# Optimization experiments

Hardware: AMD Instinct MI355X
Metric: run time of the kernel (lower is better)

## Reference

```python
import jax, jax.numpy as jnp
import numpy as np
import math

B, A, D = 32, 100, 10000
HID = 256
NH = 4
OUT = 10000
NFREQ = 16
E = round(OUT * 0.5 / (A / 2))  # max_entries = 100
N = int(math.sqrt(D))           # 100 (row/col decode of flat index)
SCALE = math.sqrt(HID)
STEPS = 3


def swish(x):
    return x * jax.nn.sigmoid(x)


def setup_inputs() -> dict:
    key = jax.random.key(0)
    ks = jax.random.split(key, 16)
    s = 0.02
    p = lambda k, shape: jax.random.normal(k, shape, jnp.float32) * s
    vals = jax.random.normal(ks[0], (B, A, D), jnp.float32)
    keep = jax.random.uniform(ks[1], (B, A, D)) < (E / D)  # ~E nonzeros per (b, agent)
    x = vals * keep
    return {
        "x": x,
        "fourier_B": jax.random.normal(ks[2], (NFREQ, 2), jnp.float32),
        "enc_W1": p(ks[3], (HID, 1 + 2 * NFREQ)), "enc_b1": jnp.zeros((HID,), jnp.float32),
        "enc_W2": p(ks[4], (HID, HID)), "enc_b2": jnp.zeros((HID,), jnp.float32),
        "pad_token": jnp.zeros((HID,), jnp.float32),
        "comp_W1": p(ks[5], (2 * HID, E * HID)), "comp_b1": jnp.zeros((2 * HID,), jnp.float32),
        "comp_W2": p(ks[6], (HID, 2 * HID)), "comp_b2": jnp.zeros((HID,), jnp.float32),
        "connectivity": jax.random.normal(ks[7], (A, A), jnp.float32),
        "qW": p(ks[8], (NH, HID, HID)), "kW": p(ks[9], (NH, HID, HID)), "vW": p(ks[10], (NH, HID, HID)),
        "fp_W1": p(ks[11], (NH, HID, HID)), "fp_b1": jnp.zeros((NH, HID), jnp.float32),
        "fp_W2": p(ks[12], (NH, HID, HID)), "fp_b2": jnp.zeros((NH, HID), jnp.float32),
        "ln_g": jnp.ones((NH, HID), jnp.float32), "ln_b": jnp.zeros((NH, HID), jnp.float32),
        "out_W": p(ks[13], (OUT, HID)), "out_b": jnp.zeros((OUT,), jnp.float32),
    }


def reference(x, fourier_B, enc_W1, enc_b1, enc_W2, enc_b2, pad_token,
              comp_W1, comp_b1, comp_W2, comp_b2, connectivity,
              qW, kW, vW, fp_W1, fp_b1, fp_W2, fp_b2, ln_g, ln_b, out_W, out_b):
    # --- ragged gather of nonzero entries, truncated/padded to E per (b, agent) ---
    mask = x != 0                                                   # [B,A,D]
    # stable argsort puts nonzero positions first, in ascending flat-index order
    # (same order as torch .nonzero per batch row)
    idx = jnp.argsort(jnp.logical_not(mask), axis=-1, stable=True)[..., :E]  # [B,A,E]
    valid = jnp.take_along_axis(mask, idx, axis=-1)                 # [B,A,E]
    vals = jnp.take_along_axis(x, idx, axis=-1)[..., None]          # [B,A,E,1]
    coords = jnp.stack([idx // N, idx % N], axis=-1).astype(x.dtype)  # [B,A,E,2]
    # Fourier positional encoding
    proj = (2.0 * math.pi) * jnp.einsum('baec,fc->baef', coords, fourier_B)
    pos = jnp.concatenate([jnp.sin(proj), jnp.cos(proj)], axis=-1)  # [B,A,E,2F]
    feat = jnp.concatenate([vals, pos], axis=-1)                    # [B,A,E,1+2F]
    # entry encoder MLP
    e = swish(feat @ enc_W1.T + enc_b1) @ enc_W2.T + enc_b2         # [B,A,E,HID]
    e = jnp.where(valid[..., None], e, pad_token)                   # pad slots -> pad_token
    # per-agent compression of the E entry embeddings
    flat = e.reshape(B, A, E * HID)
    h = swish(flat @ comp_W1.T + comp_b1) @ comp_W2.T + comp_b2     # [B,A,HID]

    # --- message passing: multi-head dot-product GAT with learned connectivity bias ---
    conn = connectivity[None, None]                                  # broadcast [1,1,A,A]
    for _ in range(STEPS):
        Q = jnp.einsum('bai,nji->nbaj', h, qW)                      # [NH,B,A,HID]
        K = jnp.einsum('bai,nji->nbaj', h, kW)
        V = jnp.einsum('bai,nji->nbaj', h, vW)
        scores = jnp.einsum('nbaj,nbcj->nbac', Q, K) / SCALE + conn
        alpha = jax.nn.softmax(scores, axis=-1)                     # dropout p=0.0
        Hm = jnp.einsum('nbac,nbcj->nbaj', alpha, V)
        t = jnp.einsum('nbaj,nij->nbai', swish(Hm), fp_W1) + fp_b1[:, None, None, :]
        t = jnp.einsum('nbaj,nij->nbai', swish(t), fp_W2) + fp_b2[:, None, None, :]
        m = t.mean(-1, keepdims=True)
        v = ((t - m) ** 2).mean(-1, keepdims=True)
        o = (t - m) / jnp.sqrt(v + 1e-5) * ln_g[:, None, None, :] + ln_b[:, None, None, :]
        h = o.mean(0)                                               # mean over heads

    return h @ out_W.T + out_b                                      # [B,A,OUT]
```

## Files before the change

kernel.cpp:

```cpp
#include <hip/hip_runtime.h>
#include <cstdint>
#include <cstddef>

#define NBATCH 32
#define NAGENT 100
#define NDIM   10000
#define HID    256
#define NHEAD  4
#define NOUT   10000
#define NFREQ  16
#define EMAX   100
#define NBA    3200
#define KBIG   25600
#define TWO_PI 6.283185307179586476925f

typedef float  v4f  __attribute__((ext_vector_type(4)));
typedef short  v8s  __attribute__((ext_vector_type(8)));

__device__ __forceinline__ unsigned short bf_hi(float f) {
    unsigned int u = __float_as_uint(f);
    return (unsigned short)((u + 0x7FFFu + ((u >> 16) & 1u)) >> 16);
}
__device__ __forceinline__ float bf_tof(unsigned short h) {
    return __uint_as_float(((unsigned int)h) << 16);
}

__global__ __launch_bounds__(64) void k_extract(const float* __restrict__ x,
                                                int* __restrict__ idxb,
                                                float* __restrict__ valb,
                                                int* __restrict__ nvalid)
{
    const int ba = blockIdx.x;
    const float* xr = x + (size_t)ba * NDIM;
    const int lane = threadIdx.x;
    int base = 0;
    for (int c0 = 0; c0 < NDIM; c0 += 64) {
        int i = c0 + lane;
        float v = (i < NDIM) ? xr[i] : 0.0f;
        unsigned long long m = __ballot(v != 0.0f);
        if (v != 0.0f) {
            int p = base + __popcll(m & ((1ull << lane) - 1ull));
            if (p < EMAX) {
                idxb[(size_t)ba * EMAX + p] = i;
                valb[(size_t)ba * EMAX + p] = v;
            }
        }
        base += __popcll(m);
        if (base >= EMAX) break;
    }
    if (lane == 0) nvalid[ba] = base < EMAX ? base : EMAX;
}

__global__ __launch_bounds__(256) void k_g1(
    const int* __restrict__ idxb, const float* __restrict__ valb,
    const int* __restrict__ nvalid, const float* __restrict__ fourB,
    const float* __restrict__ W1, const float* __restrict__ b1,
    unsigned short* __restrict__ g1h, unsigned short* __restrict__ g1l)
{
    __shared__ float s_feat[16][36];
    __shared__ float s_w[8448];
    __shared__ float s_b1v[256];
    __shared__ int   s_idx[16];
    __shared__ int   s_valid[16];

    const int t  = threadIdx.x;
    const int g0 = blockIdx.x * 16;

    if (t < 16) {
        int g = g0 + t;
        int ba = g / 100, slot = g - ba * 100;
        int valid = (slot < nvalid[ba]) ? 1 : 0;
        s_valid[t]   = valid;
        s_idx[t]     = valid ? idxb[g] : 0;
        s_feat[t][0] = valid ? valb[g] : 0.0f;
    }
    s_b1v[t] = b1[t];
    for (int i = t; i < 8448; i += 256) s_w[i] = W1[i];
    __syncthreads();

    {
        int ent = t >> 4, f = t & 15;
        float sv = 0.0f, cv = 0.0f;
        if (s_valid[ent]) {
            int id = s_idx[ent];
            float row = (float)(id / 100);
            float col = (float)(id % 100);
            float pr = TWO_PI * (row * fourB[2 * f] + col * fourB[2 * f + 1]);
            sv = sinf(pr); cv = cosf(pr);
        }
        s_feat[ent][1 + f]  = sv;
        s_feat[ent][17 + f] = cv;
    }
    __syncthreads();

    const float* wr = &s_w[t * 33];
    for (int ent = 0; ent < 16; ++ent) {
        float a = s_b1v[t];
        #pragma unroll
        for (int c = 0; c < 33; ++c) a += s_feat[ent][c] * wr[c];
        float g = a / (1.0f + expf(-a));
        g = s_valid[ent] ? g : 0.0f;
        unsigned short h = bf_hi(g);
        unsigned short l = bf_hi(g - bf_tof(h));
        size_t o = (size_t)(g0 + ent) * 256 + t;
        g1h[o] = h;
        g1l[o] = l;
    }
}

__global__ void k_w2t(const float* __restrict__ W2, float* __restrict__ W2T)
{
    int kp = blockIdx.x, k = threadIdx.x;
    W2T[kp * 256 + k] = W2[k * 256 + kp];
}

__global__ __launch_bounds__(256) void k_wsplit(const float* __restrict__ src,
                                                unsigned short* __restrict__ hi,
                                                unsigned short* __restrict__ lo)
{
    int i = (blockIdx.x * 256 + threadIdx.x) * 4;
    float4 f = *(const float4*)(src + i);
    ushort4 h, l;
    h.x = bf_hi(f.x); l.x = bf_hi(f.x - bf_tof(h.x));
    h.y = bf_hi(f.y); l.y = bf_hi(f.y - bf_tof(h.y));
    h.z = bf_hi(f.z); l.z = bf_hi(f.z - bf_tof(h.z));
    h.w = bf_hi(f.w); l.w = bf_hi(f.w - bf_tof(h.w));
    *(ushort4*)(hi + i) = h;
    *(ushort4*)(lo + i) = l;
}

__global__ __launch_bounds__(256) void k_tables(
    const float* __restrict__ W1, const float* __restrict__ pad,
    const float* __restrict__ b2, float* __restrict__ D, float* __restrict__ E0)
{
    __shared__ float red[4];
    const int n = blockIdx.x;
    const int t = threadIdx.x, lane = t & 63, w = t >> 6;
    const float pm = pad[t] - b2[t];
    const float bb = b2[t];
    const float* wr = W1 + (size_t)n * KBIG;
    float eb = 0.0f;
    for (int s = 0; s < 100; ++s) {
        float wv = wr[s * 256 + t];
        float p = pm * wv;
        eb += bb * wv;
        #pragma unroll
        for (int o = 32; o > 0; o >>= 1) p += __shfl_down(p, o);
        if (lane == 0) red[w] = p;
        __syncthreads();
        if (t == 0) D[s * 512 + n] = red[0] + red[1] + red[2] + red[3];
        __syncthreads();
    }
    #pragma unroll
    for (int o = 32; o > 0; o >>= 1) eb += __shfl_down(eb, o);
    if (lane == 0) red[w] = eb;
    __syncthreads();
    if (t == 0) E0[n] = red[0] + red[1] + red[2] + red[3];
}

__global__ void k_suffix(const float* __restrict__ D, float* __restrict__ Corr)
{
    int n = blockIdx.x * 256 + threadIdx.x;
    float c = 0.0f;
    Corr[100 * 512 + n] = 0.0f;
    for (int s = 99; s >= 0; --s) { c += D[s * 512 + n]; Corr[s * 512 + n] = c; }
}

template<int ACT, int SPLIT>
__global__ __launch_bounds__(256) void k_gemmbf(
    const unsigned short* __restrict__ Ah, const unsigned short* __restrict__ Al,
    const unsigned short* __restrict__ Wh, const unsigned short* __restrict__ Wl,
    const float* __restrict__ bias, float* __restrict__ C,
    unsigned short* __restrict__ Ch, unsigned short* __restrict__ Cl,
    int M, int N, int K,
    long long sA, long long sW, long long sBias, long long sC)
{
    __shared__ unsigned short sA_h[4096], sA_l[4096], sW_h[4096], sW_l[4096];
    const int t = threadIdx.x;
    const int z = blockIdx.z;
    Ah += (size_t)z * sA;  Al += (size_t)z * sA;
    Wh += (size_t)z * sW;  Wl += (size_t)z * sW;
    if (SPLIT) { Ch += (size_t)z * sC; Cl += (size_t)z * sC; }
    else       { C  += (size_t)z * sC; }
    const float* bp = bias ? (bias + (size_t)z * sBias) : nullptr;
    const int bn = blockIdx.x * 128, bm = blockIdx.y * 128;
    const int lane = t & 63, w = t >> 6;
    const int wm = (w & 1) * 64, wn = (w >> 1) * 64;
    const int r0 = t >> 2, kq = (t & 3) * 8;
    const int r1 = 64 + r0;
    const uint4 zero4 = make_uint4(0u, 0u, 0u, 0u);

    const unsigned short* pA0 = Ah + (size_t)(bm + r0) * K + kq;
    const unsigned short* pA1 = Ah + (size_t)(bm + r1) * K + kq;
    const unsigned short* pa0 = Al + (size_t)(bm + r0) * K + kq;
    const unsigned short* pa1 = Al + (size_t)(bm + r1) * K + kq;
    const bool v0 = (bn + r0) < N, v1 = (bn + r1) < N;
    const unsigned short* pW0 = Wh + (size_t)(bn + r0) * K + kq;
    const unsigned short* pW1 = Wh + (size_t)(bn + r1) * K + kq;
    const unsigned short* pw0 = Wl + (size_t)(bn + r0) * K + kq;
    const unsigned short* pw1 = Wl + (size_t)(bn + r1) * K + kq;

    uint4 rA0 = *(const uint4*)pA0, rA1 = *(const uint4*)pA1;
    uint4 ra0 = *(const uint4*)pa0, ra1 = *(const uint4*)pa1;
    uint4 rW0 = v0 ? *(const uint4*)pW0 : zero4;
    uint4 rW1 = v1 ? *(const uint4*)pW1 : zero4;
    uint4 rw0 = v0 ? *(const uint4*)pw0 : zero4;
    uint4 rw1 = v1 ? *(const uint4*)pw1 : zero4;

    v4f acc[4][4] = {};
    const int i0 = (r0 * 32 + kq) ^ ((r0 & 7) << 3);
    const int i1 = (r1 * 32 + kq) ^ ((r1 & 7) << 3);
    const int KT = K >> 5;

    for (int kt = 0; kt < KT; ++kt) {
        __syncthreads();
        *(uint4*)&sA_h[i0] = rA0;  *(uint4*)&sA_h[i1] = rA1;
        *(uint4*)&sA_l[i0] = ra0;  *(uint4*)&sA_l[i1] = ra1;
        *(uint4*)&sW_h[i0] = rW0;  *(uint4*)&sW_h[i1] = rW1;
        *(uint4*)&sW_l[i0] = rw0;  *(uint4*)&sW_l[i1] = rw1;
        __syncthreads();
        if (kt + 1 < KT) {
            int o = (kt + 1) * 32;
            rA0 = *(const uint4*)(pA0 + o);  rA1 = *(const uint4*)(pA1 + o);
            ra0 = *(const uint4*)(pa0 + o);  ra1 = *(const uint4*)(pa1 + o);
            rW0 = v0 ? *(const uint4*)(pW0 + o) : zero4;
            rW1 = v1 ? *(const uint4*)(pW1 + o) : zero4;
            rw0 = v0 ? *(const uint4*)(pw0 + o) : zero4;
            rw1 = v1 ? *(const uint4*)(pw1 + o) : zero4;
        }
        const int fr = lane & 15, fq = (lane >> 4) * 8;
        v8s ahf[4], alf[4], bhf[4], blf[4];
        #pragma unroll
        for (int i = 0; i < 4; ++i) {
            int ar = wm + i * 16 + fr;
            int br = wn + i * 16 + fr;
            int ai = (ar * 32 + fq) ^ ((ar & 7) << 3);
            int bi = (br * 32 + fq) ^ ((br & 7) << 3);
            ahf[i] = *(const v8s*)&sA_h[ai];
            alf[i] = *(const v8s*)&sA_l[ai];
            bhf[i] = *(const v8s*)&sW_h[bi];
            blf[i] = *(const v8s*)&sW_l[bi];
        }
        #pragma unroll
        for (int mi = 0; mi < 4; ++mi)
            #pragma unroll
            for (int ni = 0; ni < 4; ++ni) {
                acc[mi][ni] = __builtin_amdgcn_mfma_f32_16x16x32_bf16(ahf[mi], bhf[ni], acc[mi][ni], 0, 0, 0);
                acc[mi][ni] = __builtin_amdgcn_mfma_f32_16x16x32_bf16(ahf[mi], blf[ni], acc[mi][ni], 0, 0, 0);
                acc[mi][ni] = __builtin_amdgcn_mfma_f32_16x16x32_bf16(alf[mi], bhf[ni], acc[mi][ni], 0, 0, 0);
            }
    }

    const int er = (lane >> 4) * 4, ec = lane & 15;
    #pragma unroll
    for (int mi = 0; mi < 4; ++mi)
        #pragma unroll
        for (int ni = 0; ni < 4; ++ni) {
            int m = bm + wm + mi * 16 + er;
            int n = bn + wn + ni * 16 + ec;
            if (n < N) {
                float bv = bp ? bp[n] : 0.0f;
                #pragma unroll
                for (int r = 0; r < 4; ++r) {
                    float val = acc[mi][ni][r] + bv;
                    if (ACT == 1) val = val / (1.0f + expf(-val));
                    if (SPLIT) {
                        unsigned short hv = bf_hi(val);
                        Ch[(size_t)(m + r) * N + n] = hv;
                        Cl[(size_t)(m + r) * N + n] = bf_hi(val - bf_tof(hv));
                    } else {
                        C[(size_t)(m + r) * N + n] = val;
                    }
                }
            }
        }
    (void)M;
}

__global__ __launch_bounds__(256) void k_g3mfma(
    const unsigned short* __restrict__ Ah, const unsigned short* __restrict__ Al,
    const unsigned short* __restrict__ Wh, const unsigned short* __restrict__ Wl,
    float* __restrict__ part)
{
    __shared__ unsigned short sAh[4096], sAl[4096], sWh[4096], sWl[4096];
    const int t  = threadIdx.x;
    const int hwid = blockIdx.x;
    const int wk = (hwid & 7) * 100 + (hwid >> 3);
    const int bn = (wk & 3) * 128;
    const int bm = ((wk >> 2) % 25) * 128;
    const int z  = wk / 100;
    const int lane = t & 63, w = t >> 6;
    const int wm = (w & 1) * 64, wn = (w >> 1) * 64;
    const size_t K = KBIG;
    const int r0 = t >> 2, kq = (t & 3) * 8;
    const int r1 = 64 + r0;

    const unsigned short* pA0 = Ah + (size_t)(bm + r0) * K + z * 3200 + kq;
    const unsigned short* pA1 = Ah + (size_t)(bm + r1) * K + z * 3200 + kq;
    const unsigned short* pa0 = Al + (size_t)(bm + r0) * K + z * 3200 + kq;
    const unsigned short* pa1 = Al + (size_t)(bm + r1) * K + z * 3200 + kq;
    const unsigned short* pW0 = Wh + (size_t)(bn + r0) * K + z * 3200 + kq;
    const unsigned short* pW1 = Wh + (size_t)(bn + r1) * K + z * 3200 + kq;
    const unsigned short* pw0 = Wl + (size_t)(bn + r0) * K + z * 3200 + kq;
    const unsigned short* pw1 = Wl + (size_t)(bn + r1) * K + z * 3200 + kq;

    uint4 rA0 = *(const uint4*)pA0, rA1 = *(const uint4*)pA1;
    uint4 ra0 = *(const uint4*)pa0, ra1 = *(const uint4*)pa1;
    uint4 rW0 = *(const uint4*)pW0, rW1 = *(const uint4*)pW1;
    uint4 rw0 = *(const uint4*)pw0, rw1 = *(const uint4*)pw1;

    v4f acc[4][4] = {};
    const int i0 = (r0 * 32 + kq) ^ ((r0 & 7) << 3);
    const int i1 = (r1 * 32 + kq) ^ ((r1 & 7) << 3);

    for (int kt = 0; kt < 100; ++kt) {
        __syncthreads();
        *(uint4*)&sAh[i0] = rA0;  *(uint4*)&sAh[i1] = rA1;
        *(uint4*)&sAl[i0] = ra0;  *(uint4*)&sAl[i1] = ra1;
        *(uint4*)&sWh[i0] = rW0;  *(uint4*)&sWh[i1] = rW1;
        *(uint4*)&sWl[i0] = rw0;  *(uint4*)&sWl[i1] = rw1;
        __syncthreads();
        if (kt < 99) {
            int off = (kt + 1) * 32;
            rA0 = *(const uint4*)(pA0 + off);  rA1 = *(const uint4*)(pA1 + off);
            ra0 = *(const uint4*)(pa0 + off);  ra1 = *(const uint4*)(pa1 + off);
            rW0 = *(const uint4*)(pW0 + off);  rW1 = *(const uint4*)(pW1 + off);
            rw0 = *(const uint4*)(pw0 + off);  rw1 = *(const uint4*)(pw1 + off);
        }
        const int fr = lane & 15, fq = (lane >> 4) * 8;
        v8s ah[4], al[4], bh[4], bl[4];
        #pragma unroll
        for (int i = 0; i < 4; ++i) {
            int ar = wm + i * 16 + fr;
            int br = wn + i * 16 + fr;
            int ai = (ar * 32 + fq) ^ ((ar & 7) << 3);
            int bi = (br * 32 + fq) ^ ((br & 7) << 3);
            ah[i] = *(const v8s*)&sAh[ai];
            al[i] = *(const v8s*)&sAl[ai];
            bh[i] = *(const v8s*)&sWh[bi];
            bl[i] = *(const v8s*)&sWl[bi];
        }
        #pragma unroll
        for (int mi = 0; mi < 4; ++mi)
            #pragma unroll
            for (int ni = 0; ni < 4; ++ni) {
                acc[mi][ni] = __builtin_amdgcn_mfma_f32_16x16x32_bf16(ah[mi], bh[ni], acc[mi][ni], 0, 0, 0);
                acc[mi][ni] = __builtin_amdgcn_mfma_f32_16x16x32_bf16(ah[mi], bl[ni], acc[mi][ni], 0, 0, 0);
                acc[mi][ni] = __builtin_amdgcn_mfma_f32_16x16x32_bf16(al[mi], bh[ni], acc[mi][ni], 0, 0, 0);
            }
    }

    const int er = (lane >> 4) * 4, ec = lane & 15;
    float* cp = part + (size_t)z * NBA * 512;
    #pragma unroll
    for (int mi = 0; mi < 4; ++mi)
        #pragma unroll
        for (int ni = 0; ni < 4; ++ni) {
            int m = bm + wm + mi * 16 + er;
            int n = bn + wn + ni * 16 + ec;
            #pragma unroll
            for (int r = 0; r < 4; ++r)
                cp[(size_t)(m + r) * 512 + n] = acc[mi][ni][r];
        }
}

__global__ __launch_bounds__(256) void k_g3red(
    const float* __restrict__ part, const float* __restrict__ comp_b1,
    const float* __restrict__ E0, const float* __restrict__ Corr,
    const int* __restrict__ nvalid,
    unsigned short* __restrict__ oh, unsigned short* __restrict__ ol)
{
    const int i4 = (blockIdx.x * 256 + threadIdx.x) * 4;
    const int ba = i4 >> 9, n = i4 & 511;
    const size_t S = (size_t)NBA * 512;
    float4 s = *(const float4*)(part + i4);
    #pragma unroll
    for (int zz = 1; zz < 8; ++zz) {
        float4 p = *(const float4*)(part + zz * S + i4);
        s.x += p.x; s.y += p.y; s.z += p.z; s.w += p.w;
    }
    int nv = nvalid[ba];
    float4 b  = *(const float4*)(comp_b1 + n);
    float4 e  = *(const float4*)(E0 + n);
    float4 c  = *(const float4*)(Corr + nv * 512 + n);
    float r0 = s.x + b.x + e.x + c.x;
    float r1 = s.y + b.y + e.y + c.y;
    float r2 = s.z + b.z + e.z + c.z;
    float r3 = s.w + b.w + e.w + c.w;
    float4 o;
    o.x = r0 / (1.0f + expf(-r0));
    o.y = r1 / (1.0f + expf(-r1));
    o.z = r2 / (1.0f + expf(-r2));
    o.w = r3 / (1.0f + expf(-r3));
    ushort4 h, l;
    h.x = bf_hi(o.x); l.x = bf_hi(o.x - bf_tof(h.x));
    h.y = bf_hi(o.y); l.y = bf_hi(o.y - bf_tof(h.y));
    h.z = bf_hi(o.z); l.z = bf_hi(o.z - bf_tof(h.z));
    h.w = bf_hi(o.w); l.w = bf_hi(o.w - bf_tof(h.w));
    *(ushort4*)(oh + i4) = h;
    *(ushort4*)(ol + i4) = l;
}

__global__ __launch_bounds__(256) void k_attn(
    const float* __restrict__ Qb, const float* __restrict__ Kb,
    const float* __restrict__ Vb, const float* __restrict__ conn,
    unsigned short* __restrict__ Oh, unsigned short* __restrict__ Ol)
{
    __shared__ float sKV[256][101];
    __shared__ float sAl[50][100];
    __shared__ float sQ[2][256];
    __shared__ float sRed[2][2];

    const int t = threadIdx.x;
    const int half = blockIdx.x, b = blockIdx.y, n = blockIdx.z;
    const size_t base = ((size_t)n * NBA + b * 100) * 256;

    const float* Kp = Kb + base;
    for (int r = 0; r < 100; ++r) sKV[t][r] = Kp[(size_t)r * 256 + t];
    __syncthreads();

    const float* Qp = Qb + base;
    const int pair = t >> 7, tt = t & 127, lane = t & 63, wvi = t >> 6;

    for (int rr = 0; rr < 25; ++rr) {
        const int row0 = half * 50 + rr * 2;
        const int lr = rr * 2 + pair;
        __syncthreads();
        sQ[0][t] = Qp[(size_t)(row0)*256 + t];
        sQ[1][t] = Qp[(size_t)(row0 + 1) * 256 + t];
        __syncthreads();
        float sc = 0.0f;
        if (tt < 100) {
            const float* qr = sQ[pair];
            float p0 = 0.f, p1 = 0.f, p2 = 0.f, p3 = 0.f;
            #pragma unroll 4
            for (int c = 0; c < 256; c += 4) {
                p0 += qr[c]     * sKV[c][tt];
                p1 += qr[c + 1] * sKV[c + 1][tt];
                p2 += qr[c + 2] * sKV[c + 2][tt];
                p3 += qr[c + 3] * sKV[c + 3][tt];
            }
            sc = ((p0 + p1) + (p2 + p3)) * 0.0625f + conn[(row0 + pair) * 100 + tt];
            sAl[lr][tt] = sc;
        }
        __syncthreads();
        if ((wvi & 1) == 0) {
            int p = wvi >> 1;
            int r2 = rr * 2 + p;
            float m = sAl[r2][lane];
            if (lane < 36) m = fmaxf(m, sAl[r2][lane + 64]);
            #pragma unroll
            for (int off = 32; off > 0; off >>= 1)
                m = fmaxf(m, __shfl_down(m, off));
            if (lane == 0) sRed[0][p] = m;
        }
        __syncthreads();
        float ex = 0.0f;
        if (tt < 100) {
            ex = expf(sc - sRed[0][pair]);
            sAl[lr][tt] = ex;
        }
        __syncthreads();
        if ((wvi & 1) == 0) {
            int p = wvi >> 1;
            int r2 = rr * 2 + p;
            float s = sAl[r2][lane];
            if (lane < 36) s += sAl[r2][lane + 64];
            #pragma unroll
            for (int off = 32; off > 0; off >>= 1)
                s += __shfl_down(s, off);
            if (lane == 0) sRed[1][p] = s;
        }
        __syncthreads();
        if (tt < 100) sAl[lr][tt] = ex / sRed[1][pair];
    }
    __syncthreads();

    const float* Vp = Vb + base;
    for (int r = 0; r < 100; ++r) sKV[t][r] = Vp[(size_t)r * 256 + t];
    __syncthreads();

    for (int rr = 0; rr < 50; ++rr) {
        int row = half * 50 + rr;
        float a = 0.0f;
        #pragma unroll 4
        for (int j = 0; j < 100; ++j) a += sAl[rr][j] * sKV[t][j];
        float sw = a / (1.0f + expf(-a));
        size_t oidx = base + (size_t)row * 256 + t;
        unsigned short hv = bf_hi(sw);
        Oh[oidx] = hv;
        Ol[oidx] = bf_hi(sw - bf_tof(hv));
    }
}

__global__ __launch_bounds__(256) void k_ln_mean(
    const float* __restrict__ t2b, const float* __restrict__ ln_g,
    const float* __restrict__ ln_b,
    unsigned short* __restrict__ hh, unsigned short* __restrict__ hl)
{
    __shared__ float so[4][256];
    const int ba = blockIdx.x, t = threadIdx.x;
    const int n = t >> 6, lane = t & 63;
    const float* tr = t2b + ((size_t)n * NBA + ba) * HID;
    float4 v = *(const float4*)(tr + lane * 4);
    float s1 = v.x + v.y + v.z + v.w;
    float s2 = v.x * v.x + v.y * v.y + v.z * v.z + v.w * v.w;
    #pragma unroll
    for (int off = 32; off > 0; off >>= 1) {
        s1 += __shfl_down(s1, off);
        s2 += __shfl_down(s2, off);
    }
    s1 = __shfl(s1, 0);
    s2 = __shfl(s2, 0);
    float m = s1 * (1.0f / 256.0f);
    float var = s2 * (1.0f / 256.0f) - m * m;
    float rstd = 1.0f / sqrtf(var + 1e-5f);
    float4 gv = *(const float4*)(ln_g + n * HID + lane * 4);
    float4 bv = *(const float4*)(ln_b + n * HID + lane * 4);
    float4 o;
    o.x = (v.x - m) * rstd * gv.x + bv.x;
    o.y = (v.y - m) * rstd * gv.y + bv.y;
    o.z = (v.z - m) * rstd * gv.z + bv.z;
    o.w = (v.w - m) * rstd * gv.w + bv.w;
    *(float4*)&so[n][lane * 4] = o;
    __syncthreads();
    float hv = 0.25f * (so[0][t] + so[1][t] + so[2][t] + so[3][t]);
    unsigned short hi = bf_hi(hv);
    size_t oidx = (size_t)ba * HID + t;
    hh[oidx] = hi;
    hl[oidx] = bf_hi(hv - bf_tof(hi));
}

extern "C" void kernel_launch(void* const* d_in, const int* in_sizes, int n_in,
                              void* d_out, int out_size, void* d_ws, size_t ws_size,
                              hipStream_t stream)
{
    const float* x       = (const float*)d_in[0];
    const float* fourB   = (const float*)d_in[1];
    const float* enc_W1  = (const float*)d_in[2];
    const float* enc_b1  = (const float*)d_in[3];
    const float* enc_W2  = (const float*)d_in[4];
    const float* enc_b2  = (const float*)d_in[5];
    const float* pad_tok = (const float*)d_in[6];
    const float* comp_W1 = (const float*)d_in[7];
    const float* comp_b1 = (const float*)d_in[8];
    const float* comp_W2 = (const float*)d_in[9];
    const float* comp_b2 = (const float*)d_in[10];
    const float* conn    = (const float*)d_in[11];
    const float* qW      = (const float*)d_in[12];
    const float* kW      = (const float*)d_in[13];
    const float* vW      = (const float*)d_in[14];
    const float* fpW1    = (const float*)d_in[15];
    const float* fpb1    = (const float*)d_in[16];
    const float* fpW2    = (const float*)d_in[17];
    const float* fpb2    = (const float*)d_in[18];
    const float* ln_g    = (const float*)d_in[19];
    const float* ln_b    = (const float*)d_in[20];
    const float* out_W   = (const float*)d_in[21];
    const float* out_b   = (const float*)d_in[22];
    float* outp = (float*)d_out;

    char* ws = (char*)d_ws;
    size_t off = 0;
    auto alloc = [&](size_t bytes) -> void* {
        void* p = (void*)(ws + off);
        off += (bytes + 255) & ~(size_t)255;
        return p;
    };
    int*   idxb = (int*)  alloc((size_t)NBA * EMAX * 4);
    float* valb = (float*)alloc((size_t)NBA * EMAX * 4);
    int*   nval = (int*)  alloc((size_t)NBA * 4);
    unsigned short* g1h = (unsigned short*)alloc((size_t)NBA * KBIG * 2);
    unsigned short* g1l = (unsigned short*)alloc((size_t)NBA * KBIG * 2);
    float* W2T  = (float*)alloc((size_t)256 * 256 * 4);
    float* W1p  = (float*)alloc((size_t)512 * KBIG * 4);
    float* part = W1p;
    unsigned short* Whi = (unsigned short*)alloc((size_t)512 * KBIG * 2);
    unsigned short* Wlo = (unsigned short*)alloc((size_t)512 * KBIG * 2);
    float* Dt   = (float*)alloc((size_t)100 * 512 * 4);
    float* Corr = (float*)alloc((size_t)101 * 512 * 4);
    float* E0   = (float*)alloc((size_t)512 * 4);
    float* Qb   = (float*)alloc((size_t)NHEAD * NBA * HID * 4);
    float* Kb   = (float*)alloc((size_t)NHEAD * NBA * HID * 4);
    float* Vb   = (float*)alloc((size_t)NHEAD * NBA * HID * 4);
    unsigned short* asplh = (unsigned short*)alloc((size_t)NHEAD * NBA * HID * 2);
    unsigned short* aspll = (unsigned short*)alloc((size_t)NHEAD * NBA * HID * 2);
    unsigned short* cW1h = (unsigned short*)Qb;
    unsigned short* cW1l = (unsigned short*)Vb;
    unsigned short* bsplh = g1h;
    unsigned short* bspll = g1h + (size_t)NHEAD * NBA * HID;
    unsigned short* w2tH = (unsigned short*)alloc((size_t)256 * 256 * 2);
    unsigned short* w2tL = (unsigned short*)alloc((size_t)256 * 256 * 2);
    unsigned short* qkvWh = (unsigned short*)alloc((size_t)3 * NHEAD * HID * HID * 2);
    unsigned short* qkvWl = (unsigned short*)alloc((size_t)3 * NHEAD * HID * HID * 2);
    unsigned short* f1Wh = (unsigned short*)alloc((size_t)NHEAD * HID * HID * 2);
    unsigned short* f1Wl = (unsigned short*)alloc((size_t)NHEAD * HID * HID * 2);
    unsigned short* f2Wh = (unsigned short*)alloc((size_t)NHEAD * HID * HID * 2);
    unsigned short* f2Wl = (unsigned short*)alloc((size_t)NHEAD * HID * HID * 2);
    unsigned short* c2Wh = (unsigned short*)alloc((size_t)HID * 512 * 2);
    unsigned short* c2Wl = (unsigned short*)alloc((size_t)HID * 512 * 2);
    unsigned short* oWh  = (unsigned short*)alloc((size_t)NOUT * HID * 2);
    unsigned short* oWl  = (unsigned short*)alloc((size_t)NOUT * HID * 2);
    float* t2b  = Vb;

    const long long sW = (long long)HID * HID;
    const long long sC = (long long)NBA * HID;

    k_extract<<<NBA, 64, 0, stream>>>(x, idxb, valb, nval);
    k_g1<<<NBA * EMAX / 16, 256, 0, stream>>>(idxb, valb, nval, fourB,
                                              enc_W1, enc_b1, g1h, g1l);

    k_w2t<<<256, 256, 0, stream>>>(enc_W2, W2T);
    k_wsplit<<<256 * 256 / 1024, 256, 0, stream>>>(W2T, w2tH, w2tL);
    k_wsplit<<<512 * KBIG / 1024, 256, 0, stream>>>(comp_W1, cW1h, cW1l);
    k_gemmbf<0, 0><<<dim3(2, 400, 1), 256, 0, stream>>>(
        cW1h, cW1l, w2tH, w2tL, nullptr, W1p, nullptr, nullptr,
        512 * EMAX, 256, 256, 0, 0, 0, 0);
    k_wsplit<<<512 * KBIG / 1024, 256, 0, stream>>>(W1p, Whi, Wlo);
    k_tables<<<512, 256, 0, stream>>>(comp_W1, pad_tok, enc_b2, Dt, E0);
    k_suffix<<<2, 256, 0, stream>>>(Dt, Corr);

    k_wsplit<<<NHEAD * 65536 / 1024, 256, 0, stream>>>(qW, qkvWh, qkvWl);
    k_wsplit<<<NHEAD * 65536 / 1024, 256, 0, stream>>>(kW, qkvWh + NHEAD * 65536, qkvWl + NHEAD * 65536);
    k_wsplit<<<NHEAD * 65536 / 1024, 256, 0, stream>>>(vW, qkvWh + 2 * NHEAD * 65536, qkvWl + 2 * NHEAD * 65536);
    k_wsplit<<<NHEAD * 65536 / 1024, 256, 0, stream>>>(fpW1, f1Wh, f1Wl);
    k_wsplit<<<NHEAD * 65536 / 1024, 256, 0, stream>>>(fpW2, f2Wh, f2Wl);
    k_wsplit<<<HID * 512 / 1024, 256, 0, stream>>>(comp_W2, c2Wh, c2Wl);
    k_wsplit<<<NOUT * HID / 1024, 256, 0, stream>>>(out_W, oWh, oWl);

    k_g3mfma<<<800, 256, 0, stream>>>(g1h, g1l, Whi, Wlo, part);
    k_g3red<<<NBA * 512 / 1024, 256, 0, stream>>>(part, comp_b1, E0, Corr, nval, asplh, aspll);
    k_gemmbf<0, 1><<<dim3(2, 25, 1), 256, 0, stream>>>(
        asplh, aspll, c2Wh, c2Wl, comp_b2, nullptr, bsplh, bspll,
        NBA, HID, 512, 0, 0, 0, 0);

    for (int step = 0; step < 3; ++step) {
        k_gemmbf<0, 0><<<dim3(2, 25, 12), 256, 0, stream>>>(
            bsplh, bspll, qkvWh, qkvWl, nullptr, Qb, nullptr, nullptr,
            NBA, HID, HID, 0, sW, 0, sC);
        k_attn<<<dim3(2, NBATCH, NHEAD), 256, 0, stream>>>(Qb, Kb, Vb, conn, asplh, aspll);
        k_gemmbf<1, 1><<<dim3(2, 25, 4), 256, 0, stream>>>(
            asplh, aspll, f1Wh, f1Wl, fpb1, nullptr, bsplh, bspll,
            NBA, HID, HID, sC, sW, HID, sC);
        k_gemmbf<0, 0><<<dim3(2, 25, 4), 256, 0, stream>>>(
            bsplh, bspll, f2Wh, f2Wl, fpb2, t2b, nullptr, nullptr,
            NBA, HID, HID, sC, sW, HID, sC);
        k_ln_mean<<<NBA, 256, 0, stream>>>(t2b, ln_g, ln_b, bsplh, bspll);
    }

    k_gemmbf<0, 0><<<dim3(79, 25, 1), 256, 0, stream>>>(
        bsplh, bspll, oWh, oWl, out_b, outp, nullptr, nullptr,
        NBA, NOUT, HID, 0, 0, 0, 0);

    (void)in_sizes; (void)n_in; (void)out_size; (void)ws_size;
}
```

Before: 1.905 ms.

## Use direct global-to-LDS loads with double buffering in bf16 GEMM kernels

Replaces the register-staged global loads and LDS stores in both split-bf16 GEMM kernels with global_load_lds direct transfers into a double-buffered shared tile. The next K-tile is issued while the current one is consumed, and only one barrier per iteration remains. This aims to cut VGPR pressure and LDS-store instructions and to overlap memory with MFMA work. In exchange it doubles LDS use to 64KB and drops the XOR swizzle, which risks lower occupancy and bank conflicts on fragment reads.

```diff
diff --git a/kernel.cpp b/kernel.cpp
--- a/kernel.cpp
+++ b/kernel.cpp
@@ -23,6 +23,12 @@
 }
 __device__ __forceinline__ float bf_tof(unsigned short h) {
     return __uint_as_float(((unsigned int)h) << 16);
+}
+
+__device__ __forceinline__ void gld16(const void* g, void* l) {
+    __builtin_amdgcn_global_load_lds(
+        (const __attribute__((address_space(1))) void*)g,
+        (__attribute__((address_space(3))) void*)l, 16, 0, 0);
 }
 
 __global__ __launch_bounds__(64) void k_extract(const float* __restrict__ x,
@@ -175,7 +181,7 @@
     int M, int N, int K,
     long long sA, long long sW, long long sBias, long long sC)
 {
-    __shared__ unsigned short sA_h[4096], sA_l[4096], sW_h[4096], sW_l[4096];
+    __shared__ unsigned short lds[2][4][4096];
     const int t = threadIdx.x;
     const int z = blockIdx.z;
     Ah += (size_t)z * sA;  Al += (size_t)z * sA;
@@ -186,60 +192,44 @@
     const int bn = blockIdx.x * 128, bm = blockIdx.y * 128;
     const int lane = t & 63, w = t >> 6;
     const int wm = (w & 1) * 64, wn = (w >> 1) * 64;
-    const int r0 = t >> 2, kq = (t & 3) * 8;
-    const int r1 = 64 + r0;
-    const uint4 zero4 = make_uint4(0u, 0u, 0u, 0u);
-
-    const unsigned short* pA0 = Ah + (size_t)(bm + r0) * K + kq;
-    const unsigned short* pA1 = Ah + (size_t)(bm + r1) * K + kq;
-    const unsigned short* pa0 = Al + (size_t)(bm + r0) * K + kq;
-    const unsigned short* pa1 = Al + (size_t)(bm + r1) * K + kq;
-    const bool v0 = (bn + r0) < N, v1 = (bn + r1) < N;
-    const unsigned short* pW0 = Wh + (size_t)(bn + r0) * K + kq;
-    const unsigned short* pW1 = Wh + (size_t)(bn + r1) * K + kq;
-    const unsigned short* pw0 = Wl + (size_t)(bn + r0) * K + kq;
-    const unsigned short* pw1 = Wl + (size_t)(bn + r1) * K + kq;
-
-    uint4 rA0 = *(const uint4*)pA0, rA1 = *(const uint4*)pA1;
-    uint4 ra0 = *(const uint4*)pa0, ra1 = *(const uint4*)pa1;
-    uint4 rW0 = v0 ? *(const uint4*)pW0 : zero4;
-    uint4 rW1 = v1 ? *(const uint4*)pW1 : zero4;
-    uint4 rw0 = v0 ? *(const uint4*)pw0 : zero4;
-    uint4 rw1 = v1 ? *(const uint4*)pw1 : zero4;
+
+    const int sr = w * 16 + (lane >> 2);
+    const int so = (lane & 3) * 8;
+    int rw0 = bn + sr;       if (rw0 >= N) rw0 = N - 1;
+    int rw1 = bn + 64 + sr;  if (rw1 >= N) rw1 = N - 1;
+    const unsigned short* gA0 = Ah + (size_t)(bm + sr) * K + so;
+    const unsigned short* gA1 = Ah + (size_t)(bm + 64 + sr) * K + so;
+    const unsigned short* ga0 = Al + (size_t)(bm + sr) * K + so;
+    const unsigned short* ga1 = Al + (size_t)(bm + 64 + sr) * K + so;
+    const unsigned short* gW0 = Wh + (size_t)rw0 * K + so;
+    const unsigned short* gW1 = Wh + (size_t)rw1 * K + so;
+    const unsigned short* gw0 = Wl + (size_t)rw0 * K + so;
+    const unsigned short* gw1 = Wl + (size_t)rw1 * K + so;
+    const int lb0 = w * 512;
+    const int lb1 = 2048 + w * 512;
 
     v4f acc[4][4] = {};
-    const int i0 = (r0 * 32 + kq) ^ ((r0 & 7) << 3);
-    const int i1 = (r1 * 32 + kq) ^ ((r1 & 7) << 3);
+    const int fr = lane & 15, fq = (lane >> 4) * 8;
     const int KT = K >> 5;
 
+#define STAGE_G(buf, o)                                                        \
+    gld16(gA0 + (o), &lds[buf][0][lb0]); gld16(gA1 + (o), &lds[buf][0][lb1]);  \
+    gld16(ga0 + (o), &lds[buf][1][lb0]); gld16(ga1 + (o), &lds[buf][1][lb1]);  \
+    gld16(gW0 + (o), &lds[buf][2][lb0]); gld16(gW1 + (o), &lds[buf][2][lb1]);  \
+    gld16(gw0 + (o), &lds[buf][3][lb0]); gld16(gw1 + (o), &lds[buf][3][lb1]);
+
+    STAGE_G(0, 0);
+    __syncthreads();
+    int cur = 0;
     for (int kt = 0; kt < KT; ++kt) {
-        __syncthreads();
-        *(uint4*)&sA_h[i0] = rA0;  *(uint4*)&sA_h[i1] = rA1;
-        *(uint4*)&sA_l[i0] = ra0;  *(uint4*)&sA_l[i1] = ra1;
-        *(uint4*)&sW_h[i0] = rW0;  *(uint4*)&sW_h[i1] = rW1;
-        *(uint4*)&sW_l[i0] = rw0;  *(uint4*)&sW_l[i1] = rw1;
-        __syncthreads();
-        if (kt + 1 < KT) {
-            int o = (kt + 1) * 32;
-            rA0 = *(const uint4*)(pA0 + o);  rA1 = *(const uint4*)(pA1 + o);
-            ra0 = *(const uint4*)(pa0 + o);  ra1 = *(const uint4*)(pa1 + o);
-            rW0 = v0 ? *(const uint4*)(pW0 + o) : zero4;
-            rW1 = v1 ? *(const uint4*)(pW1 + o) : zero4;
-            rw0 = v0 ? *(const uint4*)(pw0 + o) : zero4;
-            rw1 = v1 ? *(const uint4*)(pw1 + o) : zero4;
-        }
-        const int fr = lane & 15, fq = (lane >> 4) * 8;
+        if (kt + 1 < KT) { STAGE_G(cur ^ 1, (kt + 1) * 32); }
         v8s ahf[4], alf[4], bhf[4], blf[4];
         #pragma unroll
         for (int i = 0; i < 4; ++i) {
-            int ar = wm + i * 16 + fr;
-            int br = wn + i * 16 + fr;
-            int ai = (ar * 32 + fq) ^ ((ar & 7) << 3);
-            int bi = (br * 32 + fq) ^ ((br & 7) << 3);
-            ahf[i] = *(const v8s*)&sA_h[ai];
-            alf[i] = *(const v8s*)&sA_l[ai];
-            bhf[i] = *(const v8s*)&sW_h[bi];
-            blf[i] = *(const v8s*)&sW_l[bi];
+            ahf[i] = *(const v8s*)&lds[cur][0][(wm + i * 16 + fr) * 32 + fq];
+            alf[i] = *(const v8s*)&lds[cur][1][(wm + i * 16 + fr) * 32 + fq];
+            bhf[i] = *(const v8s*)&lds[cur][2][(wn + i * 16 + fr) * 32 + fq];
+            blf[i] = *(const v8s*)&lds[cur][3][(wn + i * 16 + fr) * 32 + fq];
         }
         #pragma unroll
         for (int mi = 0; mi < 4; ++mi)
@@ -249,7 +239,10 @@
                 acc[mi][ni] = __builtin_amdgcn_mfma_f32_16x16x32_bf16(ahf[mi], blf[ni], acc[mi][ni], 0, 0, 0);
                 acc[mi][ni] = __builtin_amdgcn_mfma_f32_16x16x32_bf16(alf[mi], bhf[ni], acc[mi][ni], 0, 0, 0);
             }
-    }
+        __syncthreads();
+        cur ^= 1;
+    }
+#undef STAGE_G
 
     const int er = (lane >> 4) * 4, ec = lane & 15;
     #pragma unroll
@@ -282,7 +275,7 @@
     const unsigned short* __restrict__ Wh, const unsigned short* __restrict__ Wl,
     float* __restrict__ part)
 {
-    __shared__ unsigned short sAh[4096], sAl[4096], sWh[4096], sWl[4096];
+    __shared__ unsigned short lds[2][4][4096];
     const int t  = threadIdx.x;
     const int hwid = blockIdx.x;
     const int wk = (hwid & 7) * 100 + (hwid >> 3);
@@ -292,53 +285,41 @@
     const int lane = t & 63, w = t >> 6;
     const int wm = (w & 1) * 64, wn = (w >> 1) * 64;
     const size_t K = KBIG;
-    const int r0 = t >> 2, kq = (t & 3) * 8;
-    const int r1 = 64 + r0;
-
-    const unsigned short* pA0 = Ah + (size_t)(bm + r0) * K + z * 3200 + kq;
-    const unsigned short* pA1 = Ah + (size_t)(bm + r1) * K + z * 3200 + kq;
-    const unsigned short* pa0 = Al + (size_t)(bm + r0) * K + z * 3200 + kq;
-    const unsigned short* pa1 = Al + (size_t)(bm + r1) * K + z * 3200 + kq;
-    const unsigned short* pW0 = Wh + (size_t)(bn + r0) * K + z * 3200 + kq;
-    const unsigned short* pW1 = Wh + (size_t)(bn + r1) * K + z * 3200 + kq;
-    const unsigned short* pw0 = Wl + (size_t)(bn + r0) * K + z * 3200 + kq;
-    const unsigned short* pw1 = Wl + (size_t)(bn + r1) * K + z * 3200 + kq;
-
-    uint4 rA0 = *(const uint4*)pA0, rA1 = *(const uint4*)pA1;
-    uint4 ra0 = *(const uint4*)pa0, ra1 = *(const uint4*)pa1;
-    uint4 rW0 = *(const uint4*)pW0, rW1 = *(const uint4*)pW1;
-    uint4 rw0 = *(const uint4*)pw0, rw1 = *(const uint4*)pw1;
+
+    const int sr = w * 16 + (lane >> 2);
+    const int so = (lane & 3) * 8;
+    const size_t zo = (size_t)z * 3200 + so;
+    const unsigned short* gA0 = Ah + (size_t)(bm + sr) * K + zo;
+    const unsigned short* gA1 = Ah + (size_t)(bm + 64 + sr) * K + zo;
+    const unsigned short* ga0 = Al + (size_t)(bm + sr) * K + zo;
+    const unsigned short* ga1 = Al + (size_t)(bm + 64 + sr) * K + zo;
+    const unsigned short* gW0 = Wh + (size_t)(bn + sr) * K + zo;
+    const unsigned short* gW1 = Wh + (size_t)(bn + 64 + sr) * K + zo;
+    const unsigned short* gw0 = Wl + (size_t)(bn + sr) * K + zo;
+    const unsigned short* gw1 = Wl + (size_t)(bn + 64 + sr) * K + zo;
+    const int lb0 = w * 512, lb1 = 2048 + w * 512;
 
     v4f acc[4][4] = {};
-    const int i0 = (r0 * 32 + kq) ^ ((r0 & 7) << 3);
-    const int i1 = (r1 * 32 + kq) ^ ((r1 & 7) << 3);
-
+    const int fr = lane & 15, fq = (lane >> 4) * 8;
+
+#define STAGE_Z(buf, o)                                                        \
+    gld16(gA0 + (o), &lds[buf][0][lb0]); gld16(gA1 + (o), &lds[buf][0][lb1]);  \
+    gld16(ga0 + (o), &lds[buf][1][lb0]); gld16(ga1 + (o), &lds[buf][1][lb1]);  \
+    gld16(gW0 + (o), &lds[buf][2][lb0]); gld16(gW1 + (o), &lds[buf][2][lb1]);  \
+    gld16(gw0 + (o), &lds[buf][3][lb0]); gld16(gw1 + (o), &lds[buf][3][lb1]);
+
+    STAGE_Z(0, 0);
+    __syncthreads();
+    int cur = 0;
     for (int kt = 0; kt < 100; ++kt) {
-        __syncthreads();
-        *(uint4*)&sAh[i0] = rA0;  *(uint4*)&sAh[i1] = rA1;
-        *(uint4*)&sAl[i0] = ra0;  *(uint4*)&sAl[i1] = ra1;
-        *(uint4*)&sWh[i0] = rW0;  *(uint4*)&sWh[i1] = rW1;
-        *(uint4*)&sWl[i0] = rw0;  *(uint4*)&sWl[i1] = rw1;
-        __syncthreads();
-        if (kt < 99) {
-            int off = (kt + 1) * 32;
-            rA0 = *(const uint4*)(pA0 + off);  rA1 = *(const uint4*)(pA1 + off);
-            ra0 = *(const uint4*)(pa0 + off);  ra1 = *(const uint4*)(pa1 + off);
-            rW0 = *(const uint4*)(pW0 + off);  rW1 = *(const uint4*)(pW1 + off);
-            rw0 = *(const uint4*)(pw0 + off);  rw1 = *(const uint4*)(pw1 + off);
-        }
-        const int fr = lane & 15, fq = (lane >> 4) * 8;
+        if (kt < 99) { STAGE_Z(cur ^ 1, (kt + 1) * 32); }
         v8s ah[4], al[4], bh[4], bl[4];
         #pragma unroll
         for (int i = 0; i < 4; ++i) {
-            int ar = wm + i * 16 + fr;
-            int br = wn + i * 16 + fr;
-            int ai = (ar * 32 + fq) ^ ((ar & 7) << 3);
-            int bi = (br * 32 + fq) ^ ((br & 7) << 3);
-            ah[i] = *(const v8s*)&sAh[ai];
-            al[i] = *(const v8s*)&sAl[ai];
-            bh[i] = *(const v8s*)&sWh[bi];
-            bl[i] = *(const v8s*)&sWl[bi];
+            ah[i] = *(const v8s*)&lds[cur][0][(wm + i * 16 + fr) * 32 + fq];
+            al[i] = *(const v8s*)&lds[cur][1][(wm + i * 16 + fr) * 32 + fq];
+            bh[i] = *(const v8s*)&lds[cur][2][(wn + i * 16 + fr) * 32 + fq];
+            bl[i] = *(const v8s*)&lds[cur][3][(wn + i * 16 + fr) * 32 + fq];
         }
         #pragma unroll
         for (int mi = 0; mi < 4; ++mi)
@@ -348,7 +329,10 @@
                 acc[mi][ni] = __builtin_amdgcn_mfma_f32_16x16x32_bf16(ah[mi], bl[ni], acc[mi][ni], 0, 0, 0);
                 acc[mi][ni] = __builtin_amdgcn_mfma_f32_16x16x32_bf16(al[mi], bh[ni], acc[mi][ni], 0, 0, 0);
             }
-    }
+        __syncthreads();
+        cur ^= 1;
+    }
+#undef STAGE_Z
 
     const int er = (lane >> 4) * 4, ec = lane & 15;
     float* cp = part + (size_t)z * NBA * 512;
```

After: 1.825 ms. 4.2% less time.
